# Kernel optimization log

Measured on AMD Instinct MI355X. Metric: run time of the kernel, lower is better.

The kernel has to match this reference:

```python
import jax, jax.numpy as jnp
import numpy as np

SEG = 256  # segment_size from init_kwargs


def setup_inputs() -> dict:
    key = jax.random.key(0)
    ks = jax.random.split(key, 8)
    B, Lq, Lkv, D, H, dk = 2, 1024, 2048, 1024, 16, 64
    s = 1.0 / np.sqrt(D)
    return {
        "q": jax.random.normal(ks[0], (B, Lq, D), jnp.float32),
        "k": jax.random.normal(ks[1], (B, Lkv, D), jnp.float32),
        "v": jax.random.normal(ks[2], (B, Lkv, D), jnp.float32),
        "Wq": jax.random.normal(ks[3], (H, D, dk), jnp.float32) * s,
        "bq": jnp.zeros((H, dk), jnp.float32),
        "Wk": jax.random.normal(ks[4], (H, D, dk), jnp.float32) * s,
        "bk": jnp.zeros((H, dk), jnp.float32),
        "Wv": jax.random.normal(ks[5], (D, dk), jnp.float32) * s,
        "bv": jnp.zeros((dk,), jnp.float32),
        "Wh": jax.random.normal(ks[6], (dk, D), jnp.float32) * s,
    }


def reference(q, k, v, Wq, bq, Wk, bk, Wv, bv, Wh):
    B, Lq, D = q.shape
    kv_len = k.shape[1]
    S = SEG
    nseg = kv_len // S  # kv_len divisible by S -> no padding branch
    H, _, dk = Wq.shape
    dv = Wv.shape[-1]

    kseg = k.reshape(B, nseg, S, D)
    vseg = v.reshape(B, nseg, S, D)

    # per-head linear projections
    qs = jnp.einsum('bqd,hdk->bhqk', q, Wq) + bq[:, None, :]            # [B,H,Lq,dk]
    kp = jnp.einsum('bnsd,hdk->bhnsk', kseg, Wk) + bk[:, None, None, :]  # [B,H,n,S,dk]
    vp = jnp.einsum('bnsd,dv->bnsv', vseg, Wv) + bv                      # [B,n,S,dv]

    scale = jnp.sqrt(jnp.asarray(dk, q.dtype))
    attn = jnp.einsum('bhqk,bhnsk->bhnqs', qs, kp) / scale               # [B,H,n,Lq,S]
    # SAME causal mask applied to every segment (no offset), as in source
    causal = jnp.triu(jnp.ones((Lq, S), bool), k=1)
    attn = jnp.where(causal, jnp.asarray(-1e9, attn.dtype), attn)
    attn = jax.nn.softmax(attn, axis=-1)

    out = jnp.einsum('bhnqs,bnsv->bhnqv', attn, vp)                      # [B,H,n,Lq,dv]

    L = nseg * Lq  # segments concatenated along query dim (segment-major)
    head = out.reshape(B, H, L, dv).transpose(0, 2, 1, 3)                # [B,L,H,dv]
    attn_out = attn.reshape(B, H, L, S).transpose(0, 2, 1, 3)            # [B,L,H,S]

    outputs = head.mean(axis=2) @ Wh                                     # [B,L,D]
    return outputs, attn_out
```

## Files before the change

### kernel.cpp

```cpp
#include <hip/hip_runtime.h>


#define B_ 2
#define LQ 1024
#define LKV 2048
#define D_ 1024
#define H_ 16
#define DK 64
#define SEGW 256
#define NSEG 8
#define LTOT 8192

typedef _Float16 f16;
typedef __attribute__((ext_vector_type(8))) _Float16 f16x8;
typedef __attribute__((ext_vector_type(4))) _Float16 f16x4;
typedef __attribute__((ext_vector_type(4))) float f32x4;

#define MFMA_F16(a, b, c) __builtin_amdgcn_mfma_f32_16x16x32_f16((a), (b), (c), 0, 0, 0)

__global__ __launch_bounds__(256) void prep_kernel(
    const float* __restrict__ Wq, const float* __restrict__ Wk,
    const float* __restrict__ Wv, const float* __restrict__ Wh,
    f16* __restrict__ WqT, f16* __restrict__ WkT, f16* __restrict__ WvT,
    f16* __restrict__ WhT) {
  __shared__ float T[32][33];
  const int bid = blockIdx.x;
  const float* src;
  f16* dst;
  int D, N, d0, n0;
  size_t soff = 0, doff = 0;
  if (bid < 2048) {
    int z = bid >> 6, inner = bid & 63;
    int h = z & 15;
    src = (z < 16) ? Wq : Wk;
    dst = (z < 16) ? WqT : WkT;
    soff = (size_t)h * (1024 * 64);
    doff = (size_t)h * (64 * 1024);
    D = 1024; N = 64;
    d0 = (inner & 31) * 32;
    n0 = (inner >> 5) * 32;
  } else if (bid < 2112) {
    int i = bid - 2048;
    src = Wv; dst = WvT; D = 1024; N = 64;
    d0 = (i & 31) * 32;
    n0 = (i >> 5) * 32;
  } else {
    int i = bid - 2112;
    src = Wh; dst = WhT; D = 64; N = 1024;
    d0 = (i & 1) * 32;
    n0 = (i >> 1) * 32;
  }
  const int c = threadIdx.x & 31, r0 = threadIdx.x >> 5;
#pragma unroll
  for (int i = 0; i < 4; ++i) {
    int r = r0 + i * 8;
    T[r][c] = src[soff + (size_t)(d0 + r) * N + n0 + c];
  }
  __syncthreads();
#pragma unroll
  for (int i = 0; i < 4; ++i) {
    int rr = r0 + i * 8;
    dst[doff + (size_t)(n0 + rr) * D + d0 + c] = (f16)T[c][rr];
  }
}

__device__ __forceinline__ void proj_body(
    const float* __restrict__ A, const f16* __restrict__ WT,
    const float* __restrict__ bias, f16* __restrict__ C, int Mb, int bshift,
    int m0, int c0, char* smem) {
  f16(*Ah)[40] = (f16(*)[40])smem;
  f16(*Bh)[40] = (f16(*)[40])(smem + 20480);
  const int tid = threadIdx.x, lane = tid & 63, w = tid >> 6;
  const int wr = w >> 1, wc = w & 1;
  const int l15 = lane & 15, l4 = lane >> 4;
  const int f4 = tid & 7, row0 = tid >> 3;
  const int u = tid & 3, cb = tid >> 2;

  f32x4 acc[4][4];
#pragma unroll
  for (int i = 0; i < 4; ++i)
#pragma unroll
    for (int j = 0; j < 4; ++j) acc[i][j] = (f32x4)0.f;

  float4 aR[4];
  f16x8 bR[2];

#define PLOAD(k0)                                                              \
  {                                                                            \
    _Pragma("unroll") for (int p = 0; p < 4; ++p) aR[p] =                      \
        *(const float4*)(A + (size_t)(m0 + row0 + p * 32) * 1024 + (k0) +      \
                         f4 * 4);                                              \
    _Pragma("unroll") for (int p = 0; p < 2; ++p) bR[p] =                      \
        *(const f16x8*)(WT + (size_t)(c0 + cb + p * 64) * 1024 + (k0) +        \
                        u * 8);                                                \
  }
#define PSTORE(bi)                                                             \
  {                                                                            \
    _Pragma("unroll") for (int p = 0; p < 4; ++p) {                            \
      f16x4 h4;                                                                \
      h4[0] = (f16)aR[p].x; h4[1] = (f16)aR[p].y;                              \
      h4[2] = (f16)aR[p].z; h4[3] = (f16)aR[p].w;                              \
      *(f16x4*)&Ah[(bi)*128 + row0 + p * 32][f4 * 4] = h4;                     \
    }                                                                          \
    _Pragma("unroll") for (int p = 0; p < 2; ++p)                              \
        *(f16x8*)&Bh[(bi)*128 + cb + p * 64][u * 8] = bR[p];                   \
  }

  PLOAD(0);
  PSTORE(0);
  __syncthreads();

#pragma unroll 2
  for (int k = 0; k < 32; ++k) {
    if (k + 1 < 32) PLOAD((k + 1) * 32);
    const int cbuf = (k & 1) * 128;
    f16x8 ah[4], bh[4];
#pragma unroll
    for (int i = 0; i < 4; ++i) {
      ah[i] = *(const f16x8*)&Ah[cbuf + wr * 64 + i * 16 + l15][l4 * 8];
      bh[i] = *(const f16x8*)&Bh[cbuf + wc * 64 + i * 16 + l15][l4 * 8];
    }
#pragma unroll
    for (int i = 0; i < 4; ++i)
#pragma unroll
      for (int j = 0; j < 4; ++j) acc[i][j] = MFMA_F16(ah[i], bh[j], acc[i][j]);
    if (k + 1 < 32) PSTORE((k + 1) & 1);
    __syncthreads();
  }
#undef PLOAD
#undef PSTORE

#pragma unroll
  for (int j = 0; j < 4; ++j) {
    int c = c0 + wc * 64 + j * 16 + l15;
    float bs = bias[c];
    int hidx = c >> 6, dk = c & 63;
#pragma unroll
    for (int i = 0; i < 4; ++i) {
#pragma unroll
      for (int r = 0; r < 4; ++r) {
        int m = m0 + wr * 64 + i * 16 + l4 * 4 + r;
        int b = m >> bshift;
        int ml = m - (b << bshift);
        C[((size_t)(b * 16 + hidx) * Mb + ml) * 64 + dk] = (f16)(acc[i][j][r] + bs);
      }
    }
  }
}

__device__ __forceinline__ void vproj_body(
    const float* __restrict__ v, const f16* __restrict__ WvT,
    const float* __restrict__ bv, f16* __restrict__ vpTg, int m0, char* smem) {
  f16(*Av)[40] = (f16(*)[40])smem;
  f16(*Bv)[40] = (f16(*)[40])(smem + 10240);
  const int tid = threadIdx.x, lane = tid & 63, w = tid >> 6;
  const int l15 = lane & 15, l4 = lane >> 4;
  const int f4 = tid & 7, row0 = tid >> 3;
  const int u = tid & 3, cb = tid >> 2;

  f32x4 acc[4];
#pragma unroll
  for (int j = 0; j < 4; ++j) acc[j] = (f32x4)0.f;

  float4 aR[2];
  f16x8 bR;

#define VLOAD(k0)                                                              \
  {                                                                            \
    _Pragma("unroll") for (int p = 0; p < 2; ++p) aR[p] =                      \
        *(const float4*)(v + (size_t)(m0 + row0 + p * 32) * 1024 + (k0) +      \
                         f4 * 4);                                              \
    bR = *(const f16x8*)(WvT + (size_t)cb * 1024 + (k0) + u * 8);              \
  }
#define VSTORE(bi)                                                             \
  {                                                                            \
    _Pragma("unroll") for (int p = 0; p < 2; ++p) {                            \
      f16x4 h4;                                                                \
      h4[0] = (f16)aR[p].x; h4[1] = (f16)aR[p].y;                              \
      h4[2] = (f16)aR[p].z; h4[3] = (f16)aR[p].w;                              \
      *(f16x4*)&Av[(bi)*64 + row0 + p * 32][f4 * 4] = h4;                      \
    }                                                                          \
    *(f16x8*)&Bv[(bi)*64 + cb][u * 8] = bR;                                    \
  }

  VLOAD(0);
  VSTORE(0);
  __syncthreads();

#pragma unroll 2
  for (int k = 0; k < 32; ++k) {
    if (k + 1 < 32) VLOAD((k + 1) * 32);
    const int cbuf = (k & 1) * 64;
    f16x8 a8 = *(const f16x8*)&Av[cbuf + w * 16 + l15][l4 * 8];
#pragma unroll
    for (int cf = 0; cf < 4; ++cf) {
      f16x8 b8 = *(const f16x8*)&Bv[cbuf + cf * 16 + l15][l4 * 8];
      acc[cf] = MFMA_F16(a8, b8, acc[cf]);
    }
    if (k + 1 < 32) VSTORE((k + 1) & 1);
    __syncthreads();
  }
#undef VLOAD
#undef VSTORE

#pragma unroll
  for (int cf = 0; cf < 4; ++cf) {
    int dv = cf * 16 + l15;
    float bvv = bv[dv];
#pragma unroll
    for (int r = 0; r < 4; ++r) {
      int m = m0 + w * 16 + l4 * 4 + r;
      int b = m >> 11, rest = m & 2047, n = rest >> 8, si = rest & 255;
      vpTg[((size_t)((b * 8 + n) * 64 + dv)) * 256 + si] = (f16)(acc[cf][r] + bvv);
    }
  }
}

__global__ __launch_bounds__(256) void proj_all_kernel(
    const float* __restrict__ q, const float* __restrict__ k,
    const float* __restrict__ v, const f16* __restrict__ WqT,
    const f16* __restrict__ WkT, const f16* __restrict__ WvT,
    const float* __restrict__ bq, const float* __restrict__ bk,
    const float* __restrict__ bv, f16* __restrict__ qs, f16* __restrict__ kp,
    f16* __restrict__ vpTg) {
  __shared__ __align__(16) char smem[40960];
  const int bid = blockIdx.x;
  if (bid < 128) {
    proj_body(q, WqT, bq, qs, 1024, 10, (bid & 15) * 128, (bid >> 4) * 128, smem);
  } else if (bid < 384) {
    int i = bid - 128;
    proj_body(k, WkT, bk, kp, 2048, 11, (i & 31) * 128, (i >> 5) * 128, smem);
  } else {
    vproj_body(v, WvT, bv, vpTg, (bid - 384) * 64, smem);
  }
}

__global__ __launch_bounds__(256, 2) void fused_attn_kernel(
    const f16* __restrict__ qs, const f16* __restrict__ kp,
    const f16* __restrict__ vpTg, float* __restrict__ attn_out,
    f16* __restrict__ mhp) {
  __shared__ __align__(16) char Kbuf[2][32768];

  const int bid = blockIdx.x;
  const int xcd = bid & 7, sub = bid >> 3;
  const int gg = xcd * 4 + (sub >> 4);
  const int qt = sub & 15;
  const int pair = gg & 15, hgIdx = gg >> 4;
  const int b = pair >> 3, n = pair & 7;
  const int q0 = qt * 64;

  const int tid = threadIdx.x, lane = tid & 63, w = tid >> 6;
  const int l15 = lane & 15, l4 = lane >> 4;

  const int laneoff =
      (lane >> 3) * 128 + (((lane & 7) * 16) ^ ((lane >> 3) << 4));

  f16x8 vfrag[8];
  {
    const f16* vb = vpTg + ((size_t)(pair * 64 + w * 16 + l15)) * 256 + l4 * 8;
#pragma unroll
    for (int kc = 0; kc < 8; ++kc) vfrag[kc] = *(const f16x8*)(vb + kc * 32);
  }

#define STAGE_K(bufIdx, h)                                                      \
  {                                                                             \
    const char* src_ = (const char*)kp +                                        \
        ((size_t)((b * 16 + (h)) * 2048 + n * 256)) * 128;                      \
    char* lds_ = &Kbuf[bufIdx][0];                                              \
    _Pragma("unroll")                                                           \
    for (int j_ = 0; j_ < 8; ++j_) {                                            \
      int ch_ = w * 8 + j_;                                                     \
      __builtin_amdgcn_global_load_lds(                                         \
          (const __attribute__((address_space(1))) unsigned int*)(src_ +        \
              ch_ * 1024 + laneoff),                                            \
          (__attribute__((address_space(3))) unsigned int*)(lds_ + ch_ * 1024), \
          16, 0, 0);                                                            \
    }                                                                           \
  }

#define LOAD_Q(h, a0, a1)                                                       \
  {                                                                             \
    const f16* qp_ = qs +                                                       \
        ((size_t)((b * 16 + (h)) * 1024 + q0 + w * 16 + l15)) * 64 + l4 * 8;    \
    a0 = *(const f16x8*)qp_;                                                    \
    a1 = *(const f16x8*)(qp_ + 32);                                             \
  }

  f16x8 qa0, qa1, qn0, qn1;
  STAGE_K(0, hgIdx * 8);
  LOAD_Q(hgIdx * 8, qa0, qa1);
  qn0 = qa0; qn1 = qa1;

  f32x4 accO[4];
#pragma unroll
  for (int i = 0; i < 4; ++i) accO[i] = (f32x4)0.f;

  asm volatile("s_waitcnt vmcnt(2)" ::: "memory");
  __builtin_amdgcn_s_barrier();

#pragma unroll 1
  for (int hh = 0; hh < 8; ++hh) {
    const int h = hgIdx * 8 + hh;
    const int cur = hh & 1;
    if (hh < 7) {
      STAGE_K(cur ^ 1, h + 1);
      LOAD_Q(h + 1, qn0, qn1);
    }

    f32x4 accS[16];
#pragma unroll
    for (int sf = 0; sf < 16; ++sf) accS[sf] = (f32x4)0.f;
    const char* Kc = &Kbuf[cur][0];
    {
      const int sw = (l15 & 7) << 4;
      __builtin_amdgcn_s_setprio(1);
#pragma unroll
      for (int sf = 0; sf < 16; ++sf) {
        const int rowb = (sf * 16 + l15) * 128;
        f16x8 b0 = *(const f16x8*)(Kc + rowb + ((l4 * 16) ^ sw));
        f16x8 b1 = *(const f16x8*)(Kc + rowb + ((64 + l4 * 16) ^ sw));
        accS[sf] = MFMA_F16(qa0, b0, accS[sf]);
        accS[sf] = MFMA_F16(qa1, b1, accS[sf]);
      }
      __builtin_amdgcn_s_setprio(0);
    }

    float inv[4];
#pragma unroll
    for (int r = 0; r < 4; ++r) {
      const int qg = q0 + w * 16 + l4 * 4 + r;
      float mx = -3.0e38f;
#pragma unroll
      for (int sf = 0; sf < 16; ++sf) {
        int s = sf * 16 + l15;
        float vv = accS[sf][r] * 0.125f;
        if (s > qg) vv = -3.0e38f;
        accS[sf][r] = vv;
        mx = fmaxf(mx, vv);
      }
      mx = fmaxf(mx, __shfl_xor(mx, 1));
      mx = fmaxf(mx, __shfl_xor(mx, 2));
      mx = fmaxf(mx, __shfl_xor(mx, 4));
      mx = fmaxf(mx, __shfl_xor(mx, 8));
      float sum = 0.f;
#pragma unroll
      for (int sf = 0; sf < 16; ++sf) {
        float e = __expf(accS[sf][r] - mx);
        accS[sf][r] = e;
        sum += e;
      }
      sum += __shfl_xor(sum, 1);
      sum += __shfl_xor(sum, 2);
      sum += __shfl_xor(sum, 4);
      sum += __shfl_xor(sum, 8);
      inv[r] = 1.0f / sum;
    }

    asm volatile("s_waitcnt lgkmcnt(0)" ::: "memory");
    __builtin_amdgcn_s_barrier();

    char* Pc = &Kbuf[cur][0];
#pragma unroll
    for (int r = 0; r < 4; ++r) {
      const int q = w * 16 + l4 * 4 + r;
      const int sw = (q & 7) << 4;
      const int rowb = q * 512;
#pragma unroll
      for (int sf = 0; sf < 16; ++sf) {
        int s = sf * 16 + l15;
        *(f16*)(Pc + rowb + ((s * 2) ^ sw)) = (f16)(accS[sf][r] * inv[r]);
      }
    }
    asm volatile("s_waitcnt lgkmcnt(0)" ::: "memory");
    __builtin_amdgcn_s_barrier();

    __builtin_amdgcn_s_setprio(1);
#pragma unroll
    for (int kc = 0; kc < 8; ++kc) {
#pragma unroll
      for (int qb = 0; qb < 4; ++qb) {
        const int q = qb * 16 + l15;
        f16x8 pa = *(const f16x8*)(Pc + q * 512 +
                                   ((kc * 64 + l4 * 16) ^ ((q & 7) << 4)));
        accO[qb] = MFMA_F16(pa, vfrag[kc], accO[qb]);
      }
    }
    __builtin_amdgcn_s_setprio(0);

    {
      const size_t base0 =
          (((size_t)b * LTOT + (size_t)n * LQ + q0) * H_ + h) * SEGW;
#pragma unroll
      for (int it = 0; it < 16; ++it) {
        const int q = w * 16 + it;
        f16x4 p4 =
            *(const f16x4*)(Pc + q * 512 + ((lane * 8) ^ ((q & 7) << 4)));
        f32x4 f;
        f[0] = (float)p4[0]; f[1] = (float)p4[1];
        f[2] = (float)p4[2]; f[3] = (float)p4[3];
        __builtin_nontemporal_store(
            f, (f32x4*)(attn_out + base0 + (size_t)q * (H_ * SEGW) + lane * 4));
      }
    }

    qa0 = qn0; qa1 = qn1;
    asm volatile("s_waitcnt lgkmcnt(0)" ::: "memory");
    asm volatile("s_waitcnt vmcnt(16)" ::: "memory");
    __builtin_amdgcn_s_barrier();
  }

  {
    f16* mp = mhp + ((size_t)hgIdx * 16384 + (size_t)pair * 1024 + q0) * 64 +
              w * 16 + l15;
    const float s16 = 1.0f / 16.0f;
#pragma unroll
    for (int qb = 0; qb < 4; ++qb)
#pragma unroll
      for (int r = 0; r < 4; ++r)
        mp[(size_t)(qb * 16 + l4 * 4 + r) * 64] = (f16)(accO[qb][r] * s16);
  }
#undef STAGE_K
#undef LOAD_Q
}

__global__ __launch_bounds__(256) void final_f16_kernel(
    const f16* __restrict__ mhp, const f16* __restrict__ WhT,
    float* __restrict__ outputs) {
  __shared__ f16 Af[64][72], Bf[128][72];
  const int m0 = blockIdx.x * 64, c0 = blockIdx.y * 128;
  const int tid = threadIdx.x, lane = tid & 63, w = tid >> 6;
  const int l15 = lane & 15, l4 = lane >> 4;
  {
    int u = tid & 7, row0 = tid >> 3;
#pragma unroll
    for (int p = 0; p < 2; ++p) {
      int r = row0 + p * 32;
      size_t mi = (size_t)(m0 + r) * 64 + u * 8;
      f16x8 a0 = *(const f16x8*)(mhp + mi);
      f16x8 a1 = *(const f16x8*)(mhp + (size_t)16384 * 64 + mi);
      *(f16x8*)&Af[r][u * 8] = a0 + a1;
    }
    int cb = tid >> 3;
#pragma unroll
    for (int p = 0; p < 4; ++p) {
      int c = cb + p * 32;
      *(f16x8*)&Bf[c][u * 8] = *(const f16x8*)(WhT + (size_t)(c0 + c) * 64 + u * 8);
    }
  }
  __syncthreads();

  f32x4 acc[8];
#pragma unroll
  for (int cf = 0; cf < 8; ++cf) acc[cf] = (f32x4)0.f;
#pragma unroll
  for (int kc = 0; kc < 2; ++kc) {
    f16x8 a8 = *(const f16x8*)&Af[w * 16 + l15][kc * 32 + l4 * 8];
#pragma unroll
    for (int cf = 0; cf < 8; ++cf) {
      f16x8 b8 = *(const f16x8*)&Bf[cf * 16 + l15][kc * 32 + l4 * 8];
      acc[cf] = MFMA_F16(a8, b8, acc[cf]);
    }
  }
#pragma unroll
  for (int cf = 0; cf < 8; ++cf)
#pragma unroll
    for (int r = 0; r < 4; ++r)
      __builtin_nontemporal_store(
          acc[cf][r], outputs + (size_t)(m0 + w * 16 + l4 * 4 + r) * 1024 + c0 +
                          cf * 16 + l15);
}

extern "C" void kernel_launch(void* const* d_in, const int* in_sizes, int n_in,
                              void* d_out, int out_size, void* d_ws,
                              size_t ws_size, hipStream_t stream) {
  const float* q  = (const float*)d_in[0];
  const float* k  = (const float*)d_in[1];
  const float* v  = (const float*)d_in[2];
  const float* Wq = (const float*)d_in[3];
  const float* bq = (const float*)d_in[4];
  const float* Wk = (const float*)d_in[5];
  const float* bk = (const float*)d_in[6];
  const float* Wv = (const float*)d_in[7];
  const float* bv = (const float*)d_in[8];
  const float* Wh = (const float*)d_in[9];

  float* outputs  = (float*)d_out;
  float* attn_out = (float*)d_out + (size_t)B_ * LTOT * D_;

  char* ws = (char*)d_ws;
  f16* WqT  = (f16*)(ws + 0);
  f16* WkT  = (f16*)(ws + (2u << 20));
  f16* WvT  = (f16*)(ws + (4u << 20));
  f16* WhT  = (f16*)(ws + (4u << 20) + 131072);
  f16* qs   = (f16*)(ws + (4u << 20) + 262144);
  f16* kp   = (f16*)((char*)qs + (4u << 20));
  f16* vpTg = (f16*)((char*)kp + (8u << 20));
  f16* mhp  = (f16*)((char*)vpTg + (1u << 19));

  prep_kernel<<<dim3(2176), 256, 0, stream>>>(Wq, Wk, Wv, Wh, WqT, WkT, WvT, WhT);
  proj_all_kernel<<<dim3(448), 256, 0, stream>>>(q, k, v, WqT, WkT, WvT, bq, bk,
                                                 bv, qs, kp, vpTg);
  fused_attn_kernel<<<dim3(512), 256, 0, stream>>>(qs, kp, vpTg, attn_out, mhp);
  final_f16_kernel<<<dim3(256, 8), 256, 0, stream>>>(mhp, WhT, outputs);
}
```

Before: 125.5 us.

## Stage epilogues through shared memory for vectorized stores; skip mask on full tiles

```diff
diff --git a/kernel.cpp b/kernel.cpp
--- a/kernel.cpp
+++ b/kernel.cpp
@@ -130,21 +130,27 @@
 #undef PLOAD
 #undef PSTORE
 
+  f16(*Cst)[136] = (f16(*)[136])smem;
 #pragma unroll
   for (int j = 0; j < 4; ++j) {
-    int c = c0 + wc * 64 + j * 16 + l15;
-    float bs = bias[c];
+    int cl = wc * 64 + j * 16 + l15;
+    float bs = bias[c0 + cl];
+#pragma unroll
+    for (int i = 0; i < 4; ++i)
+#pragma unroll
+      for (int r = 0; r < 4; ++r)
+        Cst[wr * 64 + i * 16 + l4 * 4 + r][cl] = (f16)(acc[i][j][r] + bs);
+  }
+  __syncthreads();
+#pragma unroll
+  for (int p = 0; p < 8; ++p) {
+    int row = p * 16 + (tid >> 4);
+    int col = (tid & 15) * 8;
+    f16x8 vv = *(const f16x8*)&Cst[row][col];
+    int m = m0 + row, c = c0 + col;
+    int bb = m >> bshift, ml = m - (bb << bshift);
     int hidx = c >> 6, dk = c & 63;
-#pragma unroll
-    for (int i = 0; i < 4; ++i) {
-#pragma unroll
-      for (int r = 0; r < 4; ++r) {
-        int m = m0 + wr * 64 + i * 16 + l4 * 4 + r;
-        int b = m >> bshift;
-        int ml = m - (b << bshift);
-        C[((size_t)(b * 16 + hidx) * Mb + ml) * 64 + dk] = (f16)(acc[i][j][r] + bs);
-      }
-    }
+    *(f16x8*)(C + ((size_t)(bb * 16 + hidx) * Mb + ml) * 64 + dk) = vv;
   }
 }
 
@@ -203,16 +209,22 @@
 #undef VLOAD
 #undef VSTORE
 
+  f16(*Vst)[72] = (f16(*)[72])smem;
 #pragma unroll
   for (int cf = 0; cf < 4; ++cf) {
-    int dv = cf * 16 + l15;
-    float bvv = bv[dv];
-#pragma unroll
-    for (int r = 0; r < 4; ++r) {
-      int m = m0 + w * 16 + l4 * 4 + r;
-      int b = m >> 11, rest = m & 2047, n = rest >> 8, si = rest & 255;
-      vpTg[((size_t)((b * 8 + n) * 64 + dv)) * 256 + si] = (f16)(acc[cf][r] + bvv);
-    }
+    float bvv = bv[cf * 16 + l15];
+#pragma unroll
+    for (int r = 0; r < 4; ++r)
+      Vst[cf * 16 + l15][w * 16 + l4 * 4 + r] = (f16)(acc[cf][r] + bvv);
+  }
+  __syncthreads();
+  const int b = m0 >> 11, rest = m0 & 2047, n = rest >> 8, si0 = rest & 255;
+#pragma unroll
+  for (int p = 0; p < 2; ++p) {
+    int row = p * 32 + (tid >> 3);
+    int col = (tid & 7) * 8;
+    f16x8 vv = *(const f16x8*)&Vst[row][col];
+    *(f16x8*)(vpTg + ((size_t)((b * 8 + n) * 64 + row)) * 256 + si0 + col) = vv;
   }
 }
 
@@ -330,13 +342,22 @@
     for (int r = 0; r < 4; ++r) {
       const int qg = q0 + w * 16 + l4 * 4 + r;
       float mx = -3.0e38f;
-#pragma unroll
-      for (int sf = 0; sf < 16; ++sf) {
-        int s = sf * 16 + l15;
-        float vv = accS[sf][r] * 0.125f;
-        if (s > qg) vv = -3.0e38f;
-        accS[sf][r] = vv;
-        mx = fmaxf(mx, vv);
+      if (q0 < SEGW) {
+#pragma unroll
+        for (int sf = 0; sf < 16; ++sf) {
+          int s = sf * 16 + l15;
+          float vv = accS[sf][r] * 0.125f;
+          if (s > qg) vv = -3.0e38f;
+          accS[sf][r] = vv;
+          mx = fmaxf(mx, vv);
+        }
+      } else {
+#pragma unroll
+        for (int sf = 0; sf < 16; ++sf) {
+          float vv = accS[sf][r] * 0.125f;
+          accS[sf][r] = vv;
+          mx = fmaxf(mx, vv);
+        }
       }
       mx = fmaxf(mx, __shfl_xor(mx, 1));
       mx = fmaxf(mx, __shfl_xor(mx, 2));
@@ -426,7 +447,9 @@
 __global__ __launch_bounds__(256) void final_f16_kernel(
     const f16* __restrict__ mhp, const f16* __restrict__ WhT,
     float* __restrict__ outputs) {
-  __shared__ f16 Af[64][72], Bf[128][72];
+  __shared__ __align__(16) char smemF[33792];
+  f16(*Af)[72] = (f16(*)[72])smemF;
+  f16(*Bf)[72] = (f16(*)[72])(smemF + 9216);
   const int m0 = blockIdx.x * 64, c0 = blockIdx.y * 128;
   const int tid = threadIdx.x, lane = tid & 63, w = tid >> 6;
   const int l15 = lane & 15, l4 = lane >> 4;
@@ -461,13 +484,23 @@
       acc[cf] = MFMA_F16(a8, b8, acc[cf]);
     }
   }
+  __syncthreads();
+
+  float(*Cst)[132] = (float(*)[132])smemF;
 #pragma unroll
   for (int cf = 0; cf < 8; ++cf)
 #pragma unroll
     for (int r = 0; r < 4; ++r)
-      __builtin_nontemporal_store(
-          acc[cf][r], outputs + (size_t)(m0 + w * 16 + l4 * 4 + r) * 1024 + c0 +
-                          cf * 16 + l15);
+      Cst[w * 16 + l4 * 4 + r][cf * 16 + l15] = acc[cf][r];
+  __syncthreads();
+#pragma unroll
+  for (int p = 0; p < 8; ++p) {
+    int row = p * 8 + (tid >> 5);
+    int col = (tid & 31) * 4;
+    f32x4 vv = *(const f32x4*)&Cst[row][col];
+    __builtin_nontemporal_store(
+        vv, (f32x4*)(outputs + (size_t)(m0 + row) * 1024 + c0 + col));
+  }
 }
 
 extern "C" void kernel_launch(void* const* d_in, const int* in_sizes, int n_in,
```

Measured after the change: 118.2 us. 5.8% less time.
